# Kernel optimization log

Measured on AMD Instinct MI355X. Metric: run time of the kernel, lower is better.

Reference implementation:

```python
import jax, jax.numpy as jnp
import numpy as np

B, T, NI, NH = 64, 1024, 128, 512

def setup_inputs() -> dict:
    key = jax.random.key(0)
    k1, k2, k3, k4, k5 = jax.random.split(key, 5)
    s_i = 1.0 / np.sqrt(NI)
    s_h = 1.0 / np.sqrt(NH)
    return {
        "x":  jax.random.normal(k1, (B, T, NI), dtype=jnp.float32),
        "Wi": jax.random.uniform(k2, (NH, NI), dtype=jnp.float32, minval=-s_i, maxval=s_i),
        "bi": jax.random.uniform(k3, (NH,),    dtype=jnp.float32, minval=-s_i, maxval=s_i),
        "Wh": jax.random.uniform(k4, (NH, NH), dtype=jnp.float32, minval=-s_h, maxval=s_h),
        "bh": jax.random.uniform(k5, (NH,),    dtype=jnp.float32, minval=-s_h, maxval=s_h),
    }

def reference(x, Wi, bi, Wh, bh):
    # Input contribution is independent of state: precompute for all timesteps.
    # u: [T, B, NH]
    u = jnp.tanh(jnp.einsum('bti,hi->tbh', x, Wi) + bi)

    def step(state, u_t):
        # state: [B, NH]
        new_state = u_t + jnp.tanh(state @ Wh.T + bh)
        return new_state, new_state

    init = jnp.zeros((x.shape[0], Wh.shape[0]), dtype=x.dtype)
    last, states = jax.lax.scan(step, init, u)
    # states: [T, B, NH] -> [B, T, NH]
    return jnp.transpose(states, (1, 0, 2)), last
```

## Files before the change

kernel.cpp:

```cpp
#include <hip/hip_runtime.h>
#include <stdint.h>


typedef _Float16 half8 __attribute__((ext_vector_type(8)));
typedef float    f32x4 __attribute__((ext_vector_type(4)));
typedef uint32_t u32x4 __attribute__((ext_vector_type(4)));

#define T_STEPS 1024
#define NHID    512
#define NIN     128
#define NBATCH  64
#define STATES_ELEMS (NBATCH * T_STEPS * NHID)

__device__ __forceinline__ float tanh_fast(float x) {
  float e = __expf(2.0f * x);
  return 1.0f - 2.0f * __builtin_amdgcn_rcpf(e + 1.0f);
}
__device__ __forceinline__ uint32_t f16b(float s) {
  return (uint32_t)__builtin_bit_cast(unsigned short, (_Float16)s);
}
__device__ __forceinline__ uint32_t fbits(float s) {
  return __builtin_bit_cast(uint32_t, s);
}


__device__ __forceinline__ uint32_t load1_sc0(const uint32_t* p) {
  uint32_t v;
  asm volatile("global_load_dword %0, %1, off sc0\n\t"
               "s_waitcnt vmcnt(0)"
               : "=&v"(v) : "v"(p) : "memory");
  return v;
}
__device__ __forceinline__ uint32_t load1_dev(const uint32_t* p) {
  uint32_t v;
  asm volatile("global_load_dword %0, %1, off sc0 sc1\n\t"
               "s_waitcnt vmcnt(0)"
               : "=&v"(v) : "v"(p) : "memory");
  return v;
}

__device__ __forceinline__ void load8_sc0(
    const uint32_t* p0, const uint32_t* p1, const uint32_t* p2, const uint32_t* p3,
    const uint32_t* p4, const uint32_t* p5, const uint32_t* p6, const uint32_t* p7,
    u32x4& v0, u32x4& v1, u32x4& v2, u32x4& v3,
    u32x4& v4, u32x4& v5, u32x4& v6, u32x4& v7) {
  asm volatile(
      "global_load_dwordx4 %0, %8, off sc0\n\t"
      "global_load_dwordx4 %1, %9, off sc0\n\t"
      "global_load_dwordx4 %2, %10, off sc0\n\t"
      "global_load_dwordx4 %3, %11, off sc0\n\t"
      "global_load_dwordx4 %4, %12, off sc0\n\t"
      "global_load_dwordx4 %5, %13, off sc0\n\t"
      "global_load_dwordx4 %6, %14, off sc0\n\t"
      "global_load_dwordx4 %7, %15, off sc0\n\t"
      "s_waitcnt vmcnt(0)"
      : "=&v"(v0), "=&v"(v1), "=&v"(v2), "=&v"(v3),
        "=&v"(v4), "=&v"(v5), "=&v"(v6), "=&v"(v7)
      : "v"(p0), "v"(p1), "v"(p2), "v"(p3), "v"(p4), "v"(p5), "v"(p6), "v"(p7)
      : "memory");
}

__device__ __forceinline__ void load8_dev(
    const uint32_t* p0, const uint32_t* p1, const uint32_t* p2, const uint32_t* p3,
    const uint32_t* p4, const uint32_t* p5, const uint32_t* p6, const uint32_t* p7,
    u32x4& v0, u32x4& v1, u32x4& v2, u32x4& v3,
    u32x4& v4, u32x4& v5, u32x4& v6, u32x4& v7) {
  asm volatile(
      "global_load_dwordx4 %0, %8, off sc0 sc1\n\t"
      "global_load_dwordx4 %1, %9, off sc0 sc1\n\t"
      "global_load_dwordx4 %2, %10, off sc0 sc1\n\t"
      "global_load_dwordx4 %3, %11, off sc0 sc1\n\t"
      "global_load_dwordx4 %4, %12, off sc0 sc1\n\t"
      "global_load_dwordx4 %5, %13, off sc0 sc1\n\t"
      "global_load_dwordx4 %6, %14, off sc0 sc1\n\t"
      "global_load_dwordx4 %7, %15, off sc0 sc1\n\t"
      "s_waitcnt vmcnt(0)"
      : "=&v"(v0), "=&v"(v1), "=&v"(v2), "=&v"(v3),
        "=&v"(v4), "=&v"(v5), "=&v"(v6), "=&v"(v7)
      : "v"(p0), "v"(p1), "v"(p2), "v"(p3), "v"(p4), "v"(p5), "v"(p6), "v"(p7)
      : "memory");
}

__device__ __forceinline__ void issue_u4(
    const float* p0, const float* p1, const float* p2, const float* p3,
    float& d0, float& d1, float& d2, float& d3) {
  asm volatile(
      "global_load_dword %0, %4, off\n\t"
      "global_load_dword %1, %5, off\n\t"
      "global_load_dword %2, %6, off\n\t"
      "global_load_dword %3, %7, off"
      : "=&v"(d0), "=&v"(d1), "=&v"(d2), "=&v"(d3)
      : "v"(p0), "v"(p1), "v"(p2), "v"(p3)
      : "memory");
}

__device__ __forceinline__ void store4_plain(
    uint32_t* p0, uint32_t* p1, uint32_t* p2, uint32_t* p3,
    uint32_t d0, uint32_t d1, uint32_t d2, uint32_t d3) {
  asm volatile(
      "global_store_dword %4, %0, off\n\t"
      "global_store_dword %5, %1, off\n\t"
      "global_store_dword %6, %2, off\n\t"
      "global_store_dword %7, %3, off"
      :
      : "v"(d0), "v"(d1), "v"(d2), "v"(d3),
        "v"(p0), "v"(p1), "v"(p2), "v"(p3)
      : "memory");
}

__device__ __forceinline__ void store4_dev(
    uint32_t* p0, uint32_t* p1, uint32_t* p2, uint32_t* p3,
    uint32_t d0, uint32_t d1, uint32_t d2, uint32_t d3) {
  asm volatile(
      "global_store_dword %4, %0, off sc0 sc1\n\t"
      "global_store_dword %5, %1, off sc0 sc1\n\t"
      "global_store_dword %6, %2, off sc0 sc1\n\t"
      "global_store_dword %7, %3, off sc0 sc1"
      :
      : "v"(d0), "v"(d1), "v"(d2), "v"(d3),
        "v"(p0), "v"(p1), "v"(p2), "v"(p3)
      : "memory");
}

__global__ __launch_bounds__(256) void phase1_gemm(const float* __restrict__ x,
                                                   const float* __restrict__ Wi,
                                                   const float* __restrict__ bi,
                                                   float* __restrict__ out) {
  const int tid  = threadIdx.x;
  const int wid  = tid >> 6;
  const int lane = tid & 63;
  const int quad = lane >> 4;
  const int mcol = lane & 15;
  const int r0 = blockIdx.y * 64 + wid * 16;
  const int h0 = blockIdx.x * 64;

  f32x4 acc[4] = {};
#pragma unroll
  for (int kk = 0; kk < 4; kk++) {
    const int k = kk * 32 + quad * 8;
    const f32x4* ap = (const f32x4*)(x + (size_t)(r0 + mcol) * NIN + k);
    f32x4 alo = ap[0], ahi = ap[1];
    half8 a;
#pragma unroll
    for (int j = 0; j < 4; j++) { a[j] = (_Float16)alo[j]; a[4 + j] = (_Float16)ahi[j]; }
#pragma unroll
    for (int nt = 0; nt < 4; nt++) {
      const f32x4* bp = (const f32x4*)(Wi + (size_t)(h0 + nt * 16 + mcol) * NIN + k);
      f32x4 blo = bp[0], bhi = bp[1];
      half8 b;
#pragma unroll
      for (int j = 0; j < 4; j++) { b[j] = (_Float16)blo[j]; b[4 + j] = (_Float16)bhi[j]; }
      acc[nt] = __builtin_amdgcn_mfma_f32_16x16x32_f16(a, b, acc[nt], 0, 0, 0);
    }
  }
#pragma unroll
  for (int nt = 0; nt < 4; nt++) {
    const int h = h0 + nt * 16 + mcol;
    const float bib = bi[h];
#pragma unroll
    for (int rr = 0; rr < 4; rr++) {
      const int r = r0 + quad * 4 + rr;
      out[(size_t)r * NHID + h] = tanh_fast(acc[nt][rr] + bib);
    }
  }
}

__global__ __launch_bounds__(256, 1) void phase2_scan(const float* __restrict__ Wh,
                                                      const float* __restrict__ bh,
                                                      float* out, uint32_t* exch) {
  const int tid  = threadIdx.x;
  const int wid  = tid >> 6;
  const int lane = tid & 63;
  const int quad = lane >> 4;
  const int col  = lane & 15;
  const int wg = blockIdx.x;
  const int g  = wg & 7;
  const int w  = wg >> 3;
  const int b0 = g * 8;
  const int h0 = w * 32;

  __shared__ half8 WhF[2 * 16 * 64];
  __shared__ __align__(16) uint32_t AF[4096];

  {
    const int lh = tid >> 3;
    const int k0 = (tid & 7) * 64;
    const int nt_ = lh >> 4, n_ = lh & 15;
    const float* src = Wh + (size_t)(h0 + lh) * NHID + k0;
#pragma unroll
    for (int c = 0; c < 8; c++) {
      const int k = k0 + c * 8;
      const f32x4* p = (const f32x4*)(src + c * 8);
      f32x4 lo = p[0], hi = p[1];
      half8 hb;
#pragma unroll
      for (int j = 0; j < 4; j++) { hb[j] = (_Float16)lo[j]; hb[4 + j] = (_Float16)hi[j]; }
      WhF[(nt_ * 16 + (k >> 5)) * 64 + ((k >> 3) & 3) * 16 + n_] = hb;
    }
    for (int i = tid; i < 4096; i += 256) AF[i] = 0;
  }
  __syncthreads();

  half8 WB[16];
  float bhv = 0.0f;
  if (wid < 2) {
#pragma unroll
    for (int kk = 0; kk < 16; kk++) WB[kk] = WhF[(wid * 16 + kk) * 64 + lane];
    bhv = bh[h0 + wid * 16 + col];
    __builtin_amdgcn_s_setprio(1);
  }
  uint32_t a_off[16];
  {
    const uint32_t xr = (uint32_t)((lane & 7) << 4);
#pragma unroll
    for (int kk = 0; kk < 16; kk++)
      a_off[kk] = (uint32_t)((lane & 15) * 1024) +
                  (((uint32_t)(kk * 64 + quad * 16)) ^ xr);
  }

  const int cj = (tid >= 128) ? (tid - 128) : 0;
  uint32_t wr_off[8];
#pragma unroll
  for (int i = 0; i < 8; i++)
    wr_off[i] = (uint32_t)(i * 1024) +
                (((uint32_t)(cj * 8)) ^ (uint32_t)(i << 4));
  uint32_t* const exg = exch + (size_t)g * 8192;
  const uint32_t* pc[2][8];
#pragma unroll
  for (int s = 0; s < 2; s++)
#pragma unroll
    for (int i = 0; i < 8; i++)
      pc[s][i] = exg + s * 4096 + i * 512 + cj * 4;
  const uint32_t* pq[2];
#pragma unroll
  for (int s = 0; s < 2; s++) {
    const int prow = (lane & 3) * 2;
    const int ph   = (lane >> 2) * 32 + (lane & 3) * 4;
    pq[s] = exg + s * 4096 + prow * 512 + ph;
  }

  const int hcol = h0 + wid * 16 + col;
  const int rb = quad * 4;
  uint32_t* pe[2][4];
#pragma unroll
  for (int s = 0; s < 2; s++)
#pragma unroll
    for (int r = 0; r < 4; r++)
      pe[s][r] = exg + s * 4096 + (rb + r) * 512 + hcol;
  const float* pu[4];
  uint32_t*    ps[4];
#pragma unroll
  for (int r = 0; r < 4; r++) {
    const size_t base = (size_t)(b0 + rb + r) * (T_STEPS * NHID) + hcol;
    pu[r] = out + base;
    ps[r] = (uint32_t*)(out + base);
  }

  float uA0 = 0, uA1 = 0, uA2 = 0, uA3 = 0;
  float uB0 = 0, uB1 = 0, uB2 = 0, uB3 = 0;
  if (wid < 2 && quad < 2) {
    issue_u4(pu[0], pu[1], pu[2], pu[3], uB0, uB1, uB2, uB3);
    issue_u4(pu[0] + 512, pu[1] + 512, pu[2] + 512, pu[3] + 512,
             uA0, uA1, uA2, uA3);
#pragma unroll
    for (int r = 0; r < 4; r++) pu[r] += 1024;
    asm volatile("s_waitcnt vmcnt(4)" ::: "memory");
    __builtin_amdgcn_sched_barrier(0);
    const float tb = tanh_fast(bhv);
    const float s0 = uB0 + tb, s1 = uB1 + tb, s2 = uB2 + tb, s3 = uB3 + tb;
    const uint32_t tg1 = 1u << 16;
    const uint32_t w0 = tg1 | f16b(s0), w1 = tg1 | f16b(s1),
                   w2 = tg1 | f16b(s2), w3 = tg1 | f16b(s3);
    store4_plain(pe[0][0], pe[0][1], pe[0][2], pe[0][3], w0, w1, w2, w3);
    store4_dev  (pe[0][0], pe[0][1], pe[0][2], pe[0][3], w0, w1, w2, w3);
    store4_plain(ps[0], ps[1], ps[2], ps[3],
                 fbits(s0), fbits(s1), fbits(s2), fbits(s3));
#pragma unroll
    for (int r = 0; r < 4; r++) ps[r] += 512;
  }

  auto body = [&](int t, int sp ,
                  float& c0, float& c1, float& c2, float& c3,
                  float& n0, float& n1, float& n2, float& n3) {
    if (wid >= 2) {
      const uint32_t tg = (uint32_t)t << 16;
      {
        int tries = 0;
        for (;;) {
          uint32_t v;
          if ((tries & 3) != 3) v = load1_sc0(pq[sp]);
          else                  v = load1_dev(pq[sp]);
          if (!__any((int)((v ^ tg) & 0xFFFF0000u))) break;
          if (++tries > 64) __builtin_amdgcn_s_sleep(1);
        }
      }
      u32x4 v0, v1, v2, v3, v4, v5, v6, v7;
      int btries = 0;
      for (;;) {
        if ((btries & 3) != 3)
          load8_sc0(pc[sp][0], pc[sp][1], pc[sp][2], pc[sp][3],
                    pc[sp][4], pc[sp][5], pc[sp][6], pc[sp][7],
                    v0, v1, v2, v3, v4, v5, v6, v7);
        else
          load8_dev(pc[sp][0], pc[sp][1], pc[sp][2], pc[sp][3],
                    pc[sp][4], pc[sp][5], pc[sp][6], pc[sp][7],
                    v0, v1, v2, v3, v4, v5, v6, v7);
        uint32_t bad = (v0[0] ^ tg) | (v0[1] ^ tg) | (v0[2] ^ tg) | (v0[3] ^ tg);
        bad |= (v1[0] ^ tg) | (v1[1] ^ tg) | (v1[2] ^ tg) | (v1[3] ^ tg);
        bad |= (v2[0] ^ tg) | (v2[1] ^ tg) | (v2[2] ^ tg) | (v2[3] ^ tg);
        bad |= (v3[0] ^ tg) | (v3[1] ^ tg) | (v3[2] ^ tg) | (v3[3] ^ tg);
        bad |= (v4[0] ^ tg) | (v4[1] ^ tg) | (v4[2] ^ tg) | (v4[3] ^ tg);
        bad |= (v5[0] ^ tg) | (v5[1] ^ tg) | (v5[2] ^ tg) | (v5[3] ^ tg);
        bad |= (v6[0] ^ tg) | (v6[1] ^ tg) | (v6[2] ^ tg) | (v6[3] ^ tg);
        bad |= (v7[0] ^ tg) | (v7[1] ^ tg) | (v7[2] ^ tg) | (v7[3] ^ tg);
        if (!(bad & 0xFFFF0000u)) break;
        if (++btries > 64) __builtin_amdgcn_s_sleep(1);
      }
      char* afc = (char*)AF;
#define UNPK(i, V)                                                        \
      {                                                                   \
        uint32_t plo = ((V)[1] << 16) | ((V)[0] & 0xFFFFu);               \
        uint32_t phi = ((V)[3] << 16) | ((V)[2] & 0xFFFFu);               \
        *(uint64_t*)(afc + wr_off[i]) = ((uint64_t)phi << 32) | plo;      \
      }
      UNPK(0, v0) UNPK(1, v1) UNPK(2, v2) UNPK(3, v3)
      UNPK(4, v4) UNPK(5, v5) UNPK(6, v6) UNPK(7, v7)
#undef UNPK
    } else if (quad < 2) {
      issue_u4(pu[0], pu[1], pu[2], pu[3], n0, n1, n2, n3);
#pragma unroll
      for (int r = 0; r < 4; r++) pu[r] += 512;
    }
    asm volatile("s_waitcnt lgkmcnt(0)" ::: "memory");
    __builtin_amdgcn_s_barrier();
    asm volatile("" ::: "memory");
    if (wid < 2) {
      const char* afc = (const char*)AF;
      f32x4 A0 = {0.f, 0.f, 0.f, 0.f}, A1 = {0.f, 0.f, 0.f, 0.f};
#pragma unroll
      for (int kk = 0; kk < 16; kk += 2) {
        half8 x0 = *(const half8*)(afc + a_off[kk]);
        half8 x1 = *(const half8*)(afc + a_off[kk + 1]);
        A0 = __builtin_amdgcn_mfma_f32_16x16x32_f16(x0, WB[kk], A0, 0, 0, 0);
        A1 = __builtin_amdgcn_mfma_f32_16x16x32_f16(x1, WB[kk + 1], A1, 0, 0, 0);
      }
      if (quad < 2) {
        asm volatile("s_waitcnt vmcnt(16)" ::: "memory");
        __builtin_amdgcn_sched_barrier(0);
        const float s0 = c0 + tanh_fast(A0[0] + A1[0] + bhv);
        const float s1 = c1 + tanh_fast(A0[1] + A1[1] + bhv);
        const float s2 = c2 + tanh_fast(A0[2] + A1[2] + bhv);
        const float s3 = c3 + tanh_fast(A0[3] + A1[3] + bhv);
        const uint32_t tg1 = (uint32_t)(t + 1) << 16;
        const uint32_t w0 = tg1 | f16b(s0), w1 = tg1 | f16b(s1),
                       w2 = tg1 | f16b(s2), w3 = tg1 | f16b(s3);
        const int pb = sp ^ 1;
        store4_plain(pe[pb][0], pe[pb][1], pe[pb][2], pe[pb][3], w0, w1, w2, w3);
        store4_dev  (pe[pb][0], pe[pb][1], pe[pb][2], pe[pb][3], w0, w1, w2, w3);
        store4_plain(ps[0], ps[1], ps[2], ps[3],
                     fbits(s0), fbits(s1), fbits(s2), fbits(s3));
#pragma unroll
        for (int r = 0; r < 4; r++) ps[r] += 512;
        if (t == T_STEPS - 1) {
          uint32_t* q0 = (uint32_t*)(out + (size_t)STATES_ELEMS + (size_t)(b0 + rb + 0) * NHID + hcol);
          uint32_t* q1 = (uint32_t*)(out + (size_t)STATES_ELEMS + (size_t)(b0 + rb + 1) * NHID + hcol);
          uint32_t* q2 = (uint32_t*)(out + (size_t)STATES_ELEMS + (size_t)(b0 + rb + 2) * NHID + hcol);
          uint32_t* q3 = (uint32_t*)(out + (size_t)STATES_ELEMS + (size_t)(b0 + rb + 3) * NHID + hcol);
          store4_plain(q0, q1, q2, q3, fbits(s0), fbits(s1), fbits(s2), fbits(s3));
        }
      }
    }
  };

#pragma unroll 1
  for (int t = 1; t < T_STEPS; t += 2) {
    body(t, 0, uA0, uA1, uA2, uA3, uB0, uB1, uB2, uB3);
    if (t + 1 < T_STEPS)
      body(t + 1, 1, uB0, uB1, uB2, uB3, uA0, uA1, uA2, uA3);
  }
}

extern "C" void kernel_launch(void* const* d_in, const int* in_sizes, int n_in,
                              void* d_out, int out_size, void* d_ws, size_t ws_size,
                              hipStream_t stream) {
  const float* x  = (const float*)d_in[0];
  const float* Wi = (const float*)d_in[1];
  const float* bi = (const float*)d_in[2];
  const float* Wh = (const float*)d_in[3];
  const float* bh = (const float*)d_in[4];
  float* out = (float*)d_out;
  uint32_t* exch = (uint32_t*)d_ws;

  hipLaunchKernelGGL(phase1_gemm, dim3(8, 1024), dim3(256), 0, stream, x, Wi, bi, out);
  hipLaunchKernelGGL(phase2_scan, dim3(128), dim3(256), 0, stream, Wh, bh, out, exch);
}
```

Baseline: 2.570 ms.

## Split flag mirrors into fast and slow copies, pipeline spin probes, widen MFMA chains

The exchange buffer now has a second copy at a fixed offset. The fast copy is written with sc0 stores, and a device-coherent (sc0 sc1) copy is written separately so the slow fallback loads no longer contend with the fast path on the same address. The flag spin loop keeps two probe loads in flight and waits with vmcnt(1), so polling latency overlaps. Polling waves drop priority while spinning and raise it afterwards. The MFMA reduction uses four independent accumulators instead of two to shorten dependency chains. The risks are visibility ordering between the two copies, which relies on the exchange buffer having room at SLOW_OFF, and extra store traffic.

```diff
diff --git a/kernel.cpp b/kernel.cpp
--- a/kernel.cpp
+++ b/kernel.cpp
@@ -11,6 +11,7 @@
 #define NIN     128
 #define NBATCH  64
 #define STATES_ELEMS (NBATCH * T_STEPS * NHID)
+#define SLOW_OFF 65536
 
 __device__ __forceinline__ float tanh_fast(float x) {
   float e = __expf(2.0f * x);
@@ -24,19 +25,13 @@
 }
 
 
-__device__ __forceinline__ uint32_t load1_sc0(const uint32_t* p) {
-  uint32_t v;
-  asm volatile("global_load_dword %0, %1, off sc0\n\t"
-               "s_waitcnt vmcnt(0)"
-               : "=&v"(v) : "v"(p) : "memory");
-  return v;
-}
-__device__ __forceinline__ uint32_t load1_dev(const uint32_t* p) {
-  uint32_t v;
-  asm volatile("global_load_dword %0, %1, off sc0 sc1\n\t"
-               "s_waitcnt vmcnt(0)"
-               : "=&v"(v) : "v"(p) : "memory");
-  return v;
+__device__ __forceinline__ void probe_sc0(const uint32_t* p, uint32_t& d) {
+  asm volatile("global_load_dword %0, %1, off sc0"
+               : "=&v"(d) : "v"(p) : "memory");
+}
+__device__ __forceinline__ void probe_dev(const uint32_t* p, uint32_t& d) {
+  asm volatile("global_load_dword %0, %1, off sc0 sc1"
+               : "=&v"(d) : "v"(p) : "memory");
 }
 
 __device__ __forceinline__ void load8_sc0(
@@ -102,6 +97,20 @@
       "global_store_dword %5, %1, off\n\t"
       "global_store_dword %6, %2, off\n\t"
       "global_store_dword %7, %3, off"
+      :
+      : "v"(d0), "v"(d1), "v"(d2), "v"(d3),
+        "v"(p0), "v"(p1), "v"(p2), "v"(p3)
+      : "memory");
+}
+
+__device__ __forceinline__ void store4_sc0s(
+    uint32_t* p0, uint32_t* p1, uint32_t* p2, uint32_t* p3,
+    uint32_t d0, uint32_t d1, uint32_t d2, uint32_t d3) {
+  asm volatile(
+      "global_store_dword %4, %0, off sc0\n\t"
+      "global_store_dword %5, %1, off sc0\n\t"
+      "global_store_dword %6, %2, off sc0\n\t"
+      "global_store_dword %7, %3, off sc0"
       :
       : "v"(d0), "v"(d1), "v"(d2), "v"(d3),
         "v"(p0), "v"(p1), "v"(p2), "v"(p3)
@@ -271,8 +280,9 @@
     const uint32_t tg1 = 1u << 16;
     const uint32_t w0 = tg1 | f16b(s0), w1 = tg1 | f16b(s1),
                    w2 = tg1 | f16b(s2), w3 = tg1 | f16b(s3);
-    store4_plain(pe[0][0], pe[0][1], pe[0][2], pe[0][3], w0, w1, w2, w3);
-    store4_dev  (pe[0][0], pe[0][1], pe[0][2], pe[0][3], w0, w1, w2, w3);
+    store4_sc0s(pe[0][0], pe[0][1], pe[0][2], pe[0][3], w0, w1, w2, w3);
+    store4_dev (pe[0][0] + SLOW_OFF, pe[0][1] + SLOW_OFF,
+                pe[0][2] + SLOW_OFF, pe[0][3] + SLOW_OFF, w0, w1, w2, w3);
     store4_plain(ps[0], ps[1], ps[2], ps[3],
                  fbits(s0), fbits(s1), fbits(s2), fbits(s3));
 #pragma unroll
@@ -284,16 +294,25 @@
                   float& n0, float& n1, float& n2, float& n3) {
     if (wid >= 2) {
       const uint32_t tg = (uint32_t)t << 16;
+      __builtin_amdgcn_s_setprio(0);
+      uint32_t va, vb;
       {
+        probe_sc0(pq[sp], va);
         int tries = 0;
         for (;;) {
-          uint32_t v;
-          if ((tries & 3) != 3) v = load1_sc0(pq[sp]);
-          else                  v = load1_dev(pq[sp]);
-          if (!__any((int)((v ^ tg) & 0xFFFF0000u))) break;
-          if (++tries > 64) __builtin_amdgcn_s_sleep(1);
+          probe_sc0(pq[sp], vb);
+          asm volatile("s_waitcnt vmcnt(1)" ::: "memory");
+          __builtin_amdgcn_sched_barrier(0);
+          if (!__any((int)((va ^ tg) & 0xFFFF0000u))) break;
+          if (tries & 1) probe_dev(pq[sp] + SLOW_OFF, va);
+          else           probe_sc0(pq[sp], va);
+          asm volatile("s_waitcnt vmcnt(1)" ::: "memory");
+          __builtin_amdgcn_sched_barrier(0);
+          if (!__any((int)((vb ^ tg) & 0xFFFF0000u))) break;
+          if (++tries > 128) __builtin_amdgcn_s_sleep(1);
         }
       }
+      __builtin_amdgcn_s_setprio(1);
       u32x4 v0, v1, v2, v3, v4, v5, v6, v7;
       int btries = 0;
       for (;;) {
@@ -302,9 +321,12 @@
                     pc[sp][4], pc[sp][5], pc[sp][6], pc[sp][7],
                     v0, v1, v2, v3, v4, v5, v6, v7);
         else
-          load8_dev(pc[sp][0], pc[sp][1], pc[sp][2], pc[sp][3],
-                    pc[sp][4], pc[sp][5], pc[sp][6], pc[sp][7],
+          load8_dev(pc[sp][0] + SLOW_OFF, pc[sp][1] + SLOW_OFF,
+                    pc[sp][2] + SLOW_OFF, pc[sp][3] + SLOW_OFF,
+                    pc[sp][4] + SLOW_OFF, pc[sp][5] + SLOW_OFF,
+                    pc[sp][6] + SLOW_OFF, pc[sp][7] + SLOW_OFF,
                     v0, v1, v2, v3, v4, v5, v6, v7);
+        asm volatile("" :: "v"(va), "v"(vb));
         uint32_t bad = (v0[0] ^ tg) | (v0[1] ^ tg) | (v0[2] ^ tg) | (v0[3] ^ tg);
         bad |= (v1[0] ^ tg) | (v1[1] ^ tg) | (v1[2] ^ tg) | (v1[3] ^ tg);
         bad |= (v2[0] ^ tg) | (v2[1] ^ tg) | (v2[2] ^ tg) | (v2[3] ^ tg);
@@ -337,26 +359,33 @@
     if (wid < 2) {
       const char* afc = (const char*)AF;
       f32x4 A0 = {0.f, 0.f, 0.f, 0.f}, A1 = {0.f, 0.f, 0.f, 0.f};
-#pragma unroll
-      for (int kk = 0; kk < 16; kk += 2) {
+      f32x4 A2 = {0.f, 0.f, 0.f, 0.f}, A3 = {0.f, 0.f, 0.f, 0.f};
+#pragma unroll
+      for (int kk = 0; kk < 16; kk += 4) {
         half8 x0 = *(const half8*)(afc + a_off[kk]);
         half8 x1 = *(const half8*)(afc + a_off[kk + 1]);
-        A0 = __builtin_amdgcn_mfma_f32_16x16x32_f16(x0, WB[kk], A0, 0, 0, 0);
+        half8 x2 = *(const half8*)(afc + a_off[kk + 2]);
+        half8 x3 = *(const half8*)(afc + a_off[kk + 3]);
+        A0 = __builtin_amdgcn_mfma_f32_16x16x32_f16(x0, WB[kk],     A0, 0, 0, 0);
         A1 = __builtin_amdgcn_mfma_f32_16x16x32_f16(x1, WB[kk + 1], A1, 0, 0, 0);
+        A2 = __builtin_amdgcn_mfma_f32_16x16x32_f16(x2, WB[kk + 2], A2, 0, 0, 0);
+        A3 = __builtin_amdgcn_mfma_f32_16x16x32_f16(x3, WB[kk + 3], A3, 0, 0, 0);
       }
       if (quad < 2) {
+        const f32x4 As = (A0 + A1) + (A2 + A3);
         asm volatile("s_waitcnt vmcnt(16)" ::: "memory");
         __builtin_amdgcn_sched_barrier(0);
-        const float s0 = c0 + tanh_fast(A0[0] + A1[0] + bhv);
-        const float s1 = c1 + tanh_fast(A0[1] + A1[1] + bhv);
-        const float s2 = c2 + tanh_fast(A0[2] + A1[2] + bhv);
-        const float s3 = c3 + tanh_fast(A0[3] + A1[3] + bhv);
+        const float s0 = c0 + tanh_fast(As[0] + bhv);
+        const float s1 = c1 + tanh_fast(As[1] + bhv);
+        const float s2 = c2 + tanh_fast(As[2] + bhv);
+        const float s3 = c3 + tanh_fast(As[3] + bhv);
         const uint32_t tg1 = (uint32_t)(t + 1) << 16;
         const uint32_t w0 = tg1 | f16b(s0), w1 = tg1 | f16b(s1),
                        w2 = tg1 | f16b(s2), w3 = tg1 | f16b(s3);
         const int pb = sp ^ 1;
-        store4_plain(pe[pb][0], pe[pb][1], pe[pb][2], pe[pb][3], w0, w1, w2, w3);
-        store4_dev  (pe[pb][0], pe[pb][1], pe[pb][2], pe[pb][3], w0, w1, w2, w3);
+        store4_sc0s(pe[pb][0], pe[pb][1], pe[pb][2], pe[pb][3], w0, w1, w2, w3);
+        store4_dev (pe[pb][0] + SLOW_OFF, pe[pb][1] + SLOW_OFF,
+                    pe[pb][2] + SLOW_OFF, pe[pb][3] + SLOW_OFF, w0, w1, w2, w3);
         store4_plain(ps[0], ps[1], ps[2], ps[3],
                      fbits(s0), fbits(s1), fbits(s2), fbits(s3));
 #pragma unroll
```

Result: slower. 3.294 ms (+28.1%).
